# Optimization experiments

Measured on AMD Instinct MI355X. Metric: run time of the kernel, lower is better.

## Reference

```python
import jax, jax.numpy as jnp
import numpy as np

B, D_IN, T = 16, 512, 4096
N_CB, K, D_CB = 9, 1024, 8
EPS = 1e-12  # F.normalize eps


def setup_inputs() -> dict:
    key = jax.random.key(0)
    ks = jax.random.split(key, 8)
    z = jax.random.normal(ks[0], (B, D_IN, T), dtype=jnp.float32)
    # weight-norm params: weight = g * v / ||v|| (norm over all dims except out-channel)
    in_v = jax.random.normal(ks[1], (N_CB, D_CB, D_IN), dtype=jnp.float32) * 0.05
    in_g = jax.random.uniform(ks[2], (N_CB, D_CB), minval=0.5, maxval=1.5, dtype=jnp.float32)
    in_b = jax.random.normal(ks[3], (N_CB, D_CB), dtype=jnp.float32) * 0.01
    out_v = jax.random.normal(ks[4], (N_CB, D_IN, D_CB), dtype=jnp.float32) * 0.05
    out_g = jax.random.uniform(ks[5], (N_CB, D_IN), minval=0.5, maxval=1.5, dtype=jnp.float32)
    out_b = jax.random.normal(ks[6], (N_CB, D_IN), dtype=jnp.float32) * 0.01
    codebooks = jax.random.normal(ks[7], (N_CB, K, D_CB), dtype=jnp.float32)
    return dict(z=z, in_v=in_v, in_g=in_g, in_b=in_b,
                out_v=out_v, out_g=out_g, out_b=out_b, codebooks=codebooks)


def _wn_weight(g, v):
    # weight_norm over dim=0: normalize each output row of v
    return g[:, None] * v / jnp.linalg.norm(v, axis=1, keepdims=True)


def reference(z, in_v, in_g, in_b, out_v, out_g, out_b, codebooks):
    def step(carry, p):
        residual, latent, closs, bloss = carry
        ivi, igi, ibi, ovi, ogi, obi, cb = p
        # in_proj (1x1 conv == channel matmul)
        W_in = _wn_weight(igi, ivi)                               # [d_cb, d_in]
        z_e = jnp.einsum('oc,bct->bot', W_in, residual) + ibi[None, :, None]  # [b, d_cb, t]
        enc = z_e.transpose(0, 2, 1).reshape(B * T, D_CB)         # (b t) d
        enc_n = enc / jnp.maximum(jnp.linalg.norm(enc, axis=1, keepdims=True), EPS)
        cb_n = cb / jnp.maximum(jnp.linalg.norm(cb, axis=1, keepdims=True), EPS)
        # squared L2 distance between normalized vectors
        dist = ((enc_n * enc_n).sum(1, keepdims=True)
                - 2.0 * enc_n @ cb_n.T
                + (cb_n * cb_n).sum(1)[None, :])                  # [(b t), K]
        idx = jnp.argmin(dist, axis=1).reshape(B, T)              # [b, t]
        z_q = cb[idx].transpose(0, 2, 1)                          # [b, d_cb, t] (raw codebook)
        # losses: per-batch mean over [1,2], then mean over batch == global mean (eval mask all True)
        closs = closs + ((z_e - jax.lax.stop_gradient(z_q)) ** 2).mean()
        bloss = bloss + ((z_q - jax.lax.stop_gradient(z_e)) ** 2).mean()
        # straight-through estimator
        z_q_st = z_e + jax.lax.stop_gradient(z_q - z_e)
        W_out = _wn_weight(ogi, ovi)                              # [d_in, d_cb]
        lat_i = jnp.einsum('oc,bct->bot', W_out, z_q_st) + obi[None, :, None]  # [b, d_in, t]
        latent = latent + lat_i
        residual = residual - lat_i
        return (residual, latent, closs, bloss), idx

    init = (z, jnp.zeros_like(z), jnp.float32(0.0), jnp.float32(0.0))
    xs = (in_v, in_g, in_b, out_v, out_g, out_b, codebooks)
    (_, latent, closs, bloss), indices = jax.lax.scan(step, init, xs)
    codes = indices.transpose(1, 0, 2)  # [b, n_codebooks, t]
    return codes, latent, closs, bloss
```

## Files before the change

### kernel.cpp

```cpp
#include <hip/hip_runtime.h>
#include <hip/hip_bf16.h>

constexpr int NB  = 16;
constexpr int DIN = 512;
constexpr int TT  = 4096;
constexpr int NCB = 9;
constexpr int KK  = 1024;

constexpr size_t OUT_LAT   = (size_t)NB * NCB * TT;
constexpr size_t OUT_CLOSS = OUT_LAT + (size_t)NB * DIN * TT;

constexpr int SRES = 514;
constexpr int SWIN = 516;

__device__ __align__(16) float g_cbn [NCB * KK * 8];
__device__ __align__(16) float g_c2  [NCB * KK];
__device__ __align__(16) float g_win [NCB * 8 * DIN];
__device__ __align__(16) float g_wout[NCB * DIN * 8];
__device__ double g_loss;

__device__ __forceinline__ float sqf(float x) {
  float r = x * x;
  asm volatile("" : "+v"(r));
  return r;
}

__global__ void prep_win_k(const float* __restrict__ in_v, const float* __restrict__ in_g) {
  const int r = blockIdx.x * 64 + threadIdx.x;
  if (r >= NCB * 8) return;
  const float* v = in_v + (size_t)r * DIN;
  float blk[4];
#pragma unroll
  for (int bb = 0; bb < 4; ++bb) {
    const float* a = v + bb * 128;
    float r8[8];
#pragma unroll
    for (int j = 0; j < 8; ++j) r8[j] = sqf(a[j]);
#pragma unroll
    for (int m = 1; m < 16; ++m)
#pragma unroll
      for (int j = 0; j < 8; ++j) r8[j] += sqf(a[m * 8 + j]);
    blk[bb] = ((r8[0] + r8[1]) + (r8[2] + r8[3])) + ((r8[4] + r8[5]) + (r8[6] + r8[7]));
  }
  const float total = (blk[0] + blk[1]) + (blk[2] + blk[3]);
  const float nrm = sqrtf(total);
  const float g = in_g[r];
  float* w = g_win + (size_t)r * DIN;
  for (int c = 0; c < DIN; ++c) w[c] = (g * v[c]) / nrm;
}

__global__ void prep_wout_k(const float* __restrict__ out_v, const float* __restrict__ out_g) {
  const int row = blockIdx.x * 256 + threadIdx.x;
  const float* v = out_v + (size_t)row * 8;
  float q[8];
#pragma unroll
  for (int d = 0; d < 8; ++d) q[d] = sqf(v[d]);
  const float nrm = sqrtf(((q[0] + q[1]) + (q[2] + q[3])) + ((q[4] + q[5]) + (q[6] + q[7])));
  const float g = out_g[row];
  float* w = g_wout + (size_t)row * 8;
#pragma unroll
  for (int d = 0; d < 8; ++d) w[d] = (g * v[d]) / nrm;
}

__global__ void prep_cbn_k(const float* __restrict__ cb) {
  const int row = blockIdx.x * 256 + threadIdx.x;
  const float* v = cb + (size_t)row * 8;
  float q[8];
#pragma unroll
  for (int d = 0; d < 8; ++d) q[d] = sqf(v[d]);
  float nrm = sqrtf(((q[0] + q[1]) + (q[2] + q[3])) + ((q[4] + q[5]) + (q[6] + q[7])));
  nrm = fmaxf(nrm, 1e-12f);
  float cn[8];
#pragma unroll
  for (int d = 0; d < 8; ++d) { cn[d] = v[d] / nrm; g_cbn[(size_t)row * 8 + d] = cn[d]; }
  float s2[8];
#pragma unroll
  for (int d = 0; d < 8; ++d) s2[d] = sqf(cn[d]);
  g_c2[row] = ((s2[0] + s2[1]) + (s2[2] + s2[3])) + ((s2[4] + s2[5]) + (s2[6] + s2[7]));
  if (row == 0) g_loss = 0.0;
}

__global__ __launch_bounds__(256, 3)
void rvq_main_k(const float* __restrict__ z, const float* __restrict__ in_b,
                const float* __restrict__ out_b, const float* __restrict__ cb,
                float* __restrict__ out) {
  __shared__ __align__(16) float s_res[16 * SRES];
  __shared__ __align__(16) float s_win[8 * SWIN];
  __shared__ float s_ze[128];
  __shared__ float s_en[128];
  __shared__ float s_s[16];
  __shared__ float s_cd[256];
  __shared__ int   s_ck[256];
  __shared__ float s_zq[128];

  const int tid = threadIdx.x;
  const int col = tid & 15;
  const int grp = tid >> 4;
  const int b   = blockIdx.x >> 8;
  const int t0  = (blockIdx.x & 255) << 4;

  float lr[32];
  {
    const float* zb = z + (size_t)b * DIN * TT + t0 + col;
#pragma unroll
    for (int j = 0; j < 32; ++j) {
      const int c = grp + (j << 4);
      s_res[col * SRES + c] = zb[(size_t)c * TT];
      lr[j] = 0.0f;
    }
  }

  float loss_acc = 0.0f;

  for (int i = 0; i < NCB; ++i) {
    {
      const float4* gw = (const float4*)(g_win + i * 4096);
#pragma unroll
      for (int q = 0; q < 4; ++q) {
        const int e = (q * 256 + tid) * 4;
        *(float4*)(s_win + (e >> 9) * SWIN + (e & 511)) = gw[q * 256 + tid];
      }
    }
    __syncthreads();

    if (tid < 128) {
      const int o = tid >> 4, cc = tid & 15;
      const float2* wr = (const float2*)(s_win + o * SWIN);
      const float2* rr = (const float2*)(s_res + cc * SRES);
      float acc = 0.0f;
#pragma unroll 8
      for (int h = 0; h < 256; ++h) {
        const float2 w = wr[h];
        const float2 r = rr[h];
        acc = fmaf(w.x, r.x, acc);
        acc = fmaf(w.y, r.y, acc);
      }
      s_ze[o * 16 + cc] = acc + in_b[i * 8 + o];
    }
    __syncthreads();

    if (tid < 16) {
      float e[8], q[8];
#pragma unroll
      for (int d = 0; d < 8; ++d) { e[d] = s_ze[d * 16 + tid]; q[d] = sqf(e[d]); }
      float nrm = sqrtf(((q[0] + q[1]) + (q[2] + q[3])) + ((q[4] + q[5]) + (q[6] + q[7])));
      nrm = fmaxf(nrm, 1e-12f);
      float en[8], s2[8];
#pragma unroll
      for (int d = 0; d < 8; ++d) { en[d] = e[d] / nrm; s_en[d * 16 + tid] = en[d]; s2[d] = sqf(en[d]); }
      s_s[tid] = ((s2[0] + s2[1]) + (s2[2] + s2[3])) + ((s2[4] + s2[5]) + (s2[6] + s2[7]));
    }
    __syncthreads();

    {
      const float en0 = s_en[0 * 16 + col], en1 = s_en[1 * 16 + col];
      const float en2 = s_en[2 * 16 + col], en3 = s_en[3 * 16 + col];
      const float en4 = s_en[4 * 16 + col], en5 = s_en[5 * 16 + col];
      const float en6 = s_en[6 * 16 + col], en7 = s_en[7 * 16 + col];
      const float sv = s_s[col];
      const float* cp  = g_cbn + (size_t)i * 8192 + (grp << 3);
      const float* c2p = g_c2 + i * KK + grp;
      float dmin = 3.402823466e38f; int kmin = 0;
#pragma unroll 4
      for (int j = 0; j < 64; ++j) {
        const float4 c0 = *(const float4*)(cp + (j << 7));
        const float4 c1 = *(const float4*)(cp + (j << 7) + 4);
        const float cc2 = c2p[j << 4];
        float dot = 0.0f;
        dot = fmaf(en0, c0.x, dot); dot = fmaf(en1, c0.y, dot);
        dot = fmaf(en2, c0.z, dot); dot = fmaf(en3, c0.w, dot);
        dot = fmaf(en4, c1.x, dot); dot = fmaf(en5, c1.y, dot);
        dot = fmaf(en6, c1.z, dot); dot = fmaf(en7, c1.w, dot);
        const float dist = fmaf(-2.0f, dot, sv) + cc2;
        if (dist < dmin) { dmin = dist; kmin = (j << 4) + grp; }
      }
      s_cd[grp * 16 + col] = dmin;
      s_ck[grp * 16 + col] = kmin;
    }
    __syncthreads();

    if (tid < 16) {
      float bd = s_cd[tid]; int bk = s_ck[tid];
#pragma unroll
      for (int ks = 1; ks < 16; ++ks) {
        const float d2 = s_cd[ks * 16 + tid]; const int k2 = s_ck[ks * 16 + tid];
        if (d2 < bd || (d2 == bd && k2 < bk)) { bd = d2; bk = k2; }
      }
      out[((size_t)b * NCB + i) * TT + t0 + tid] = (float)bk;
      const float* cr = cb + ((size_t)i * KK + bk) * 8;
#pragma unroll
      for (int d = 0; d < 8; ++d) {
        const float zq = cr[d];
        const float ze = s_ze[d * 16 + tid];
        const float df = ze - zq;
        loss_acc = fmaf(df, df, loss_acc);
        s_zq[d * 16 + tid] = ze + (zq - ze);
      }
    }
    __syncthreads();

    {
      const float q0 = s_zq[0 * 16 + col], q1 = s_zq[1 * 16 + col];
      const float q2 = s_zq[2 * 16 + col], q3 = s_zq[3 * 16 + col];
      const float q4 = s_zq[4 * 16 + col], q5 = s_zq[5 * 16 + col];
      const float q6 = s_zq[6 * 16 + col], q7 = s_zq[7 * 16 + col];
      const float* gw = g_wout + (size_t)i * 4096;
      const float* ob = out_b + i * DIN;
#pragma unroll 4
      for (int j = 0; j < 32; ++j) {
        const int c = grp + (j << 4);
        const float4 w0 = *(const float4*)(gw + c * 8);
        const float4 w1 = *(const float4*)(gw + c * 8 + 4);
        float dot = 0.0f;
        dot = fmaf(w0.x, q0, dot); dot = fmaf(w0.y, q1, dot);
        dot = fmaf(w0.z, q2, dot); dot = fmaf(w0.w, q3, dot);
        dot = fmaf(w1.x, q4, dot); dot = fmaf(w1.y, q5, dot);
        dot = fmaf(w1.z, q6, dot); dot = fmaf(w1.w, q7, dot);
        const float lat = dot + ob[c];
        lr[j] += lat;
        s_res[col * SRES + c] -= lat;
      }
    }
  }

  {
    float* lat = out + OUT_LAT;
#pragma unroll
    for (int j = 0; j < 32; ++j) {
      const int c = grp + (j << 4);
      lat[((size_t)b * DIN + c) * TT + t0 + col] = lr[j];
    }
  }

  if (tid < 64) {
    float v = loss_acc;
#pragma unroll
    for (int off = 32; off; off >>= 1) v += __shfl_down(v, off);
    if (tid == 0) atomicAdd(&g_loss, (double)v);
  }
}

__global__ void rvq_epi_k(float* __restrict__ out) {
  const float m = (float)(g_loss / 524288.0);
  out[OUT_CLOSS]     = m;
  out[OUT_CLOSS + 1] = m;
}

extern "C" void kernel_launch(void* const* d_in, const int* in_sizes, int n_in,
                              void* d_out, int out_size, void* d_ws, size_t ws_size,
                              hipStream_t stream) {
  const float* z     = (const float*)d_in[0];
  const float* in_v  = (const float*)d_in[1];
  const float* in_g  = (const float*)d_in[2];
  const float* in_b  = (const float*)d_in[3];
  const float* out_v = (const float*)d_in[4];
  const float* out_g = (const float*)d_in[5];
  const float* out_b = (const float*)d_in[6];
  const float* cb    = (const float*)d_in[7];
  float* out = (float*)d_out;
  (void)d_ws; (void)ws_size;

  prep_win_k <<<2, 64, 0, stream>>>(in_v, in_g);
  prep_wout_k<<<18, 256, 0, stream>>>(out_v, out_g);
  prep_cbn_k <<<36, 256, 0, stream>>>(cb);
  rvq_main_k <<<4096, 256, 0, stream>>>(z, in_b, out_b, cb, out);
  rvq_epi_k  <<<1, 1, 0, stream>>>(out);
}
```

Baseline: 1.432 ms.

## Restructure RVQ block: fewer barriers, shuffle argmin, global W_in reads, fused prep

```diff
diff --git a/kernel.cpp b/kernel.cpp
--- a/kernel.cpp
+++ b/kernel.cpp
@@ -10,8 +10,7 @@
 constexpr size_t OUT_LAT   = (size_t)NB * NCB * TT;
 constexpr size_t OUT_CLOSS = OUT_LAT + (size_t)NB * DIN * TT;
 
-constexpr int SRES = 514;
-constexpr int SWIN = 516;
+constexpr int SRES = 516;
 
 __device__ __align__(16) float g_cbn [NCB * KK * 8];
 __device__ __align__(16) float g_c2  [NCB * KK];
@@ -25,77 +24,75 @@
   return r;
 }
 
-__global__ void prep_win_k(const float* __restrict__ in_v, const float* __restrict__ in_g) {
-  const int r = blockIdx.x * 64 + threadIdx.x;
-  if (r >= NCB * 8) return;
-  const float* v = in_v + (size_t)r * DIN;
-  float blk[4];
-#pragma unroll
-  for (int bb = 0; bb < 4; ++bb) {
-    const float* a = v + bb * 128;
-    float r8[8];
-#pragma unroll
-    for (int j = 0; j < 8; ++j) r8[j] = sqf(a[j]);
-#pragma unroll
-    for (int m = 1; m < 16; ++m)
-#pragma unroll
-      for (int j = 0; j < 8; ++j) r8[j] += sqf(a[m * 8 + j]);
-    blk[bb] = ((r8[0] + r8[1]) + (r8[2] + r8[3])) + ((r8[4] + r8[5]) + (r8[6] + r8[7]));
-  }
-  const float total = (blk[0] + blk[1]) + (blk[2] + blk[3]);
-  const float nrm = sqrtf(total);
-  const float g = in_g[r];
-  float* w = g_win + (size_t)r * DIN;
-  for (int c = 0; c < DIN; ++c) w[c] = (g * v[c]) / nrm;
-}
-
-__global__ void prep_wout_k(const float* __restrict__ out_v, const float* __restrict__ out_g) {
-  const int row = blockIdx.x * 256 + threadIdx.x;
-  const float* v = out_v + (size_t)row * 8;
-  float q[8];
-#pragma unroll
-  for (int d = 0; d < 8; ++d) q[d] = sqf(v[d]);
-  const float nrm = sqrtf(((q[0] + q[1]) + (q[2] + q[3])) + ((q[4] + q[5]) + (q[6] + q[7])));
-  const float g = out_g[row];
-  float* w = g_wout + (size_t)row * 8;
-#pragma unroll
-  for (int d = 0; d < 8; ++d) w[d] = (g * v[d]) / nrm;
-}
-
-__global__ void prep_cbn_k(const float* __restrict__ cb) {
-  const int row = blockIdx.x * 256 + threadIdx.x;
-  const float* v = cb + (size_t)row * 8;
-  float q[8];
-#pragma unroll
-  for (int d = 0; d < 8; ++d) q[d] = sqf(v[d]);
-  float nrm = sqrtf(((q[0] + q[1]) + (q[2] + q[3])) + ((q[4] + q[5]) + (q[6] + q[7])));
-  nrm = fmaxf(nrm, 1e-12f);
-  float cn[8];
-#pragma unroll
-  for (int d = 0; d < 8; ++d) { cn[d] = v[d] / nrm; g_cbn[(size_t)row * 8 + d] = cn[d]; }
-  float s2[8];
-#pragma unroll
-  for (int d = 0; d < 8; ++d) s2[d] = sqf(cn[d]);
-  g_c2[row] = ((s2[0] + s2[1]) + (s2[2] + s2[3])) + ((s2[4] + s2[5]) + (s2[6] + s2[7]));
-  if (row == 0) g_loss = 0.0;
-}
-
-__global__ __launch_bounds__(256, 3)
+__global__ void prep_all_k(const float* __restrict__ in_v, const float* __restrict__ in_g,
+                           const float* __restrict__ out_v, const float* __restrict__ out_g,
+                           const float* __restrict__ cb) {
+  const int bid = blockIdx.x, tid = threadIdx.x;
+  if (bid < 36) {
+    const int row = bid * 256 + tid;
+    const float* v = cb + (size_t)row * 8;
+    float q[8];
+#pragma unroll
+    for (int d = 0; d < 8; ++d) q[d] = sqf(v[d]);
+    float nrm = sqrtf(((q[0] + q[1]) + (q[2] + q[3])) + ((q[4] + q[5]) + (q[6] + q[7])));
+    nrm = fmaxf(nrm, 1e-12f);
+    float cn[8];
+#pragma unroll
+    for (int d = 0; d < 8; ++d) { cn[d] = v[d] / nrm; g_cbn[(size_t)row * 8 + d] = cn[d]; }
+    float s2[8];
+#pragma unroll
+    for (int d = 0; d < 8; ++d) s2[d] = sqf(cn[d]);
+    g_c2[row] = ((s2[0] + s2[1]) + (s2[2] + s2[3])) + ((s2[4] + s2[5]) + (s2[6] + s2[7]));
+    if (row == 0) g_loss = 0.0;
+  } else if (bid < 54) {
+    const int row = (bid - 36) * 256 + tid;
+    const float* v = out_v + (size_t)row * 8;
+    float q[8];
+#pragma unroll
+    for (int d = 0; d < 8; ++d) q[d] = sqf(v[d]);
+    const float nrm = sqrtf(((q[0] + q[1]) + (q[2] + q[3])) + ((q[4] + q[5]) + (q[6] + q[7])));
+    const float g = out_g[row];
+    float* w = g_wout + (size_t)row * 8;
+#pragma unroll
+    for (int d = 0; d < 8; ++d) w[d] = (g * v[d]) / nrm;
+  } else {
+    const int r = tid;
+    if (r >= NCB * 8) return;
+    const float* v = in_v + (size_t)r * DIN;
+    float blk[4];
+#pragma unroll
+    for (int bb = 0; bb < 4; ++bb) {
+      const float* a = v + bb * 128;
+      float r8[8];
+#pragma unroll
+      for (int j = 0; j < 8; ++j) r8[j] = sqf(a[j]);
+#pragma unroll
+      for (int m = 1; m < 16; ++m)
+#pragma unroll
+        for (int j = 0; j < 8; ++j) r8[j] += sqf(a[m * 8 + j]);
+      blk[bb] = ((r8[0] + r8[1]) + (r8[2] + r8[3])) + ((r8[4] + r8[5]) + (r8[6] + r8[7]));
+    }
+    const float total = (blk[0] + blk[1]) + (blk[2] + blk[3]);
+    const float nrm = sqrtf(total);
+    const float g = in_g[r];
+    float* w = g_win + (size_t)r * DIN;
+    for (int c = 0; c < DIN; ++c) w[c] = (g * v[c]) / nrm;
+  }
+}
+
+__global__ __launch_bounds__(256, 4)
 void rvq_main_k(const float* __restrict__ z, const float* __restrict__ in_b,
                 const float* __restrict__ out_b, const float* __restrict__ cb,
                 float* __restrict__ out) {
   __shared__ __align__(16) float s_res[16 * SRES];
-  __shared__ __align__(16) float s_win[8 * SWIN];
   __shared__ float s_ze[128];
-  __shared__ float s_en[128];
-  __shared__ float s_s[16];
-  __shared__ float s_cd[256];
-  __shared__ int   s_ck[256];
   __shared__ float s_zq[128];
 
   const int tid = threadIdx.x;
   const int col = tid & 15;
-  const int grp = tid >> 4;
+  const int cg  = tid >> 4;
+  const int bcol = tid >> 4;
+  const int ksb  = tid & 15;
   const int b   = blockIdx.x >> 8;
   const int t0  = (blockIdx.x & 255) << 4;
 
@@ -103,140 +100,135 @@
   {
     const float* zb = z + (size_t)b * DIN * TT + t0 + col;
 #pragma unroll
-    for (int j = 0; j < 32; ++j) {
-      const int c = grp + (j << 4);
-      s_res[col * SRES + c] = zb[(size_t)c * TT];
-      lr[j] = 0.0f;
+    for (int p = 0; p < 16; ++p) {
+      const int c0 = 2 * cg + 32 * p;
+      const float v0 = zb[(size_t)c0 * TT];
+      const float v1 = zb[(size_t)(c0 + 1) * TT];
+      *(float2*)(s_res + col * SRES + c0) = make_float2(v0, v1);
+      lr[2 * p] = 0.0f; lr[2 * p + 1] = 0.0f;
     }
   }
 
   float loss_acc = 0.0f;
 
   for (int i = 0; i < NCB; ++i) {
+    __syncthreads();
+
+    if (tid < 64) {
+      const int cc = tid & 15, og = tid >> 4;
+      const float4* rr  = (const float4*)(s_res + cc * SRES);
+      const float4* w0p = (const float4*)(g_win + (size_t)(i * 8 + og) * DIN);
+      const float4* w1p = (const float4*)(g_win + (size_t)(i * 8 + og + 4) * DIN);
+      float a0 = 0.0f, a1 = 0.0f;
+#pragma unroll 4
+      for (int h = 0; h < 128; ++h) {
+        const float4 r  = rr[h];
+        const float4 w0 = w0p[h];
+        const float4 w1 = w1p[h];
+        a0 = fmaf(w0.x, r.x, a0); a0 = fmaf(w0.y, r.y, a0);
+        a0 = fmaf(w0.z, r.z, a0); a0 = fmaf(w0.w, r.w, a0);
+        a1 = fmaf(w1.x, r.x, a1); a1 = fmaf(w1.y, r.y, a1);
+        a1 = fmaf(w1.z, r.z, a1); a1 = fmaf(w1.w, r.w, a1);
+      }
+      s_ze[og * 16 + cc]       = a0 + in_b[i * 8 + og];
+      s_ze[(og + 4) * 16 + cc] = a1 + in_b[i * 8 + og + 4];
+    }
+    __syncthreads();
+
     {
-      const float4* gw = (const float4*)(g_win + i * 4096);
-#pragma unroll
-      for (int q = 0; q < 4; ++q) {
-        const int e = (q * 256 + tid) * 4;
-        *(float4*)(s_win + (e >> 9) * SWIN + (e & 511)) = gw[q * 256 + tid];
-      }
-    }
-    __syncthreads();
-
-    if (tid < 128) {
-      const int o = tid >> 4, cc = tid & 15;
-      const float2* wr = (const float2*)(s_win + o * SWIN);
-      const float2* rr = (const float2*)(s_res + cc * SRES);
-      float acc = 0.0f;
-#pragma unroll 8
-      for (int h = 0; h < 256; ++h) {
-        const float2 w = wr[h];
-        const float2 r = rr[h];
-        acc = fmaf(w.x, r.x, acc);
-        acc = fmaf(w.y, r.y, acc);
-      }
-      s_ze[o * 16 + cc] = acc + in_b[i * 8 + o];
-    }
-    __syncthreads();
-
-    if (tid < 16) {
       float e[8], q[8];
 #pragma unroll
-      for (int d = 0; d < 8; ++d) { e[d] = s_ze[d * 16 + tid]; q[d] = sqf(e[d]); }
+      for (int d = 0; d < 8; ++d) { e[d] = s_ze[d * 16 + bcol]; q[d] = sqf(e[d]); }
       float nrm = sqrtf(((q[0] + q[1]) + (q[2] + q[3])) + ((q[4] + q[5]) + (q[6] + q[7])));
       nrm = fmaxf(nrm, 1e-12f);
       float en[8], s2[8];
 #pragma unroll
-      for (int d = 0; d < 8; ++d) { en[d] = e[d] / nrm; s_en[d * 16 + tid] = en[d]; s2[d] = sqf(en[d]); }
-      s_s[tid] = ((s2[0] + s2[1]) + (s2[2] + s2[3])) + ((s2[4] + s2[5]) + (s2[6] + s2[7]));
-    }
-    __syncthreads();
-
-    {
-      const float en0 = s_en[0 * 16 + col], en1 = s_en[1 * 16 + col];
-      const float en2 = s_en[2 * 16 + col], en3 = s_en[3 * 16 + col];
-      const float en4 = s_en[4 * 16 + col], en5 = s_en[5 * 16 + col];
-      const float en6 = s_en[6 * 16 + col], en7 = s_en[7 * 16 + col];
-      const float sv = s_s[col];
-      const float* cp  = g_cbn + (size_t)i * 8192 + (grp << 3);
-      const float* c2p = g_c2 + i * KK + grp;
+      for (int d = 0; d < 8; ++d) { en[d] = e[d] / nrm; s2[d] = sqf(en[d]); }
+      const float sv = ((s2[0] + s2[1]) + (s2[2] + s2[3])) + ((s2[4] + s2[5]) + (s2[6] + s2[7]));
+
+      const float4* cp4 = (const float4*)(g_cbn + (size_t)i * 8192 + (ksb << 3));
+      const float* c2p  = g_c2 + i * KK + ksb;
       float dmin = 3.402823466e38f; int kmin = 0;
 #pragma unroll 4
       for (int j = 0; j < 64; ++j) {
-        const float4 c0 = *(const float4*)(cp + (j << 7));
-        const float4 c1 = *(const float4*)(cp + (j << 7) + 4);
+        const float4 c0 = cp4[j * 32];
+        const float4 c1 = cp4[j * 32 + 1];
         const float cc2 = c2p[j << 4];
         float dot = 0.0f;
-        dot = fmaf(en0, c0.x, dot); dot = fmaf(en1, c0.y, dot);
-        dot = fmaf(en2, c0.z, dot); dot = fmaf(en3, c0.w, dot);
-        dot = fmaf(en4, c1.x, dot); dot = fmaf(en5, c1.y, dot);
-        dot = fmaf(en6, c1.z, dot); dot = fmaf(en7, c1.w, dot);
+        dot = fmaf(en[0], c0.x, dot); dot = fmaf(en[1], c0.y, dot);
+        dot = fmaf(en[2], c0.z, dot); dot = fmaf(en[3], c0.w, dot);
+        dot = fmaf(en[4], c1.x, dot); dot = fmaf(en[5], c1.y, dot);
+        dot = fmaf(en[6], c1.z, dot); dot = fmaf(en[7], c1.w, dot);
         const float dist = fmaf(-2.0f, dot, sv) + cc2;
-        if (dist < dmin) { dmin = dist; kmin = (j << 4) + grp; }
-      }
-      s_cd[grp * 16 + col] = dmin;
-      s_ck[grp * 16 + col] = kmin;
-    }
-    __syncthreads();
-
-    if (tid < 16) {
-      float bd = s_cd[tid]; int bk = s_ck[tid];
-#pragma unroll
-      for (int ks = 1; ks < 16; ++ks) {
-        const float d2 = s_cd[ks * 16 + tid]; const int k2 = s_ck[ks * 16 + tid];
-        if (d2 < bd || (d2 == bd && k2 < bk)) { bd = d2; bk = k2; }
-      }
-      out[((size_t)b * NCB + i) * TT + t0 + tid] = (float)bk;
-      const float* cr = cb + ((size_t)i * KK + bk) * 8;
-#pragma unroll
-      for (int d = 0; d < 8; ++d) {
-        const float zq = cr[d];
-        const float ze = s_ze[d * 16 + tid];
+        if (dist < dmin) { dmin = dist; kmin = (j << 4) + ksb; }
+      }
+#pragma unroll
+      for (int m = 1; m < 16; m <<= 1) {
+        const float od = __shfl_xor(dmin, m, 16);
+        const int   ok = __shfl_xor(kmin, m, 16);
+        if (od < dmin || (od == dmin && ok < kmin)) { dmin = od; kmin = ok; }
+      }
+      if (ksb == 0) out[((size_t)b * NCB + i) * TT + t0 + bcol] = (float)kmin;
+      if (ksb < 8) {
+        const int d = ksb;
+        const float zq = cb[((size_t)i * KK + kmin) * 8 + d];
+        const float ze = s_ze[d * 16 + bcol];
         const float df = ze - zq;
         loss_acc = fmaf(df, df, loss_acc);
-        s_zq[d * 16 + tid] = ze + (zq - ze);
+        s_zq[d * 16 + bcol] = ze + (zq - ze);
       }
     }
     __syncthreads();
 
     {
-      const float q0 = s_zq[0 * 16 + col], q1 = s_zq[1 * 16 + col];
-      const float q2 = s_zq[2 * 16 + col], q3 = s_zq[3 * 16 + col];
-      const float q4 = s_zq[4 * 16 + col], q5 = s_zq[5 * 16 + col];
-      const float q6 = s_zq[6 * 16 + col], q7 = s_zq[7 * 16 + col];
+      float qv[8];
+#pragma unroll
+      for (int d = 0; d < 8; ++d) qv[d] = s_zq[d * 16 + col];
       const float* gw = g_wout + (size_t)i * 4096;
-      const float* ob = out_b + i * DIN;
+      const float2* ob2 = (const float2*)(out_b + i * DIN);
 #pragma unroll 4
-      for (int j = 0; j < 32; ++j) {
-        const int c = grp + (j << 4);
-        const float4 w0 = *(const float4*)(gw + c * 8);
-        const float4 w1 = *(const float4*)(gw + c * 8 + 4);
-        float dot = 0.0f;
-        dot = fmaf(w0.x, q0, dot); dot = fmaf(w0.y, q1, dot);
-        dot = fmaf(w0.z, q2, dot); dot = fmaf(w0.w, q3, dot);
-        dot = fmaf(w1.x, q4, dot); dot = fmaf(w1.y, q5, dot);
-        dot = fmaf(w1.z, q6, dot); dot = fmaf(w1.w, q7, dot);
-        const float lat = dot + ob[c];
-        lr[j] += lat;
-        s_res[col * SRES + c] -= lat;
+      for (int p = 0; p < 16; ++p) {
+        const int c0 = 2 * cg + 32 * p;
+        const float4 wa = *(const float4*)(gw + c0 * 8);
+        const float4 wb = *(const float4*)(gw + c0 * 8 + 4);
+        const float4 wc = *(const float4*)(gw + c0 * 8 + 8);
+        const float4 wd = *(const float4*)(gw + c0 * 8 + 12);
+        float d0 = 0.0f, d1 = 0.0f;
+        d0 = fmaf(wa.x, qv[0], d0); d0 = fmaf(wa.y, qv[1], d0);
+        d0 = fmaf(wa.z, qv[2], d0); d0 = fmaf(wa.w, qv[3], d0);
+        d0 = fmaf(wb.x, qv[4], d0); d0 = fmaf(wb.y, qv[5], d0);
+        d0 = fmaf(wb.z, qv[6], d0); d0 = fmaf(wb.w, qv[7], d0);
+        d1 = fmaf(wc.x, qv[0], d1); d1 = fmaf(wc.y, qv[1], d1);
+        d1 = fmaf(wc.z, qv[2], d1); d1 = fmaf(wc.w, qv[3], d1);
+        d1 = fmaf(wd.x, qv[4], d1); d1 = fmaf(wd.y, qv[5], d1);
+        d1 = fmaf(wd.z, qv[6], d1); d1 = fmaf(wd.w, qv[7], d1);
+        const float2 ob = ob2[cg + 16 * p];
+        const float lat0 = d0 + ob.x;
+        const float lat1 = d1 + ob.y;
+        lr[2 * p] += lat0; lr[2 * p + 1] += lat1;
+        float2* rp = (float2*)(s_res + col * SRES + c0);
+        float2 rv = *rp;
+        rv.x -= lat0; rv.y -= lat1;
+        *rp = rv;
       }
     }
   }
 
   {
-    float* lat = out + OUT_LAT;
-#pragma unroll
-    for (int j = 0; j < 32; ++j) {
-      const int c = grp + (j << 4);
-      lat[((size_t)b * DIN + c) * TT + t0 + col] = lr[j];
-    }
-  }
-
-  if (tid < 64) {
+    float* lat = out + OUT_LAT + (size_t)b * DIN * TT + t0 + col;
+#pragma unroll
+    for (int p = 0; p < 16; ++p) {
+      const int c0 = 2 * cg + 32 * p;
+      lat[(size_t)c0 * TT]       = lr[2 * p];
+      lat[(size_t)(c0 + 1) * TT] = lr[2 * p + 1];
+    }
+  }
+
+  {
     float v = loss_acc;
 #pragma unroll
     for (int off = 32; off; off >>= 1) v += __shfl_down(v, off);
-    if (tid == 0) atomicAdd(&g_loss, (double)v);
+    if ((tid & 63) == 0) atomicAdd(&g_loss, (double)v);
   }
 }
 
@@ -260,9 +252,7 @@
   float* out = (float*)d_out;
   (void)d_ws; (void)ws_size;
 
-  prep_win_k <<<2, 64, 0, stream>>>(in_v, in_g);
-  prep_wout_k<<<18, 256, 0, stream>>>(out_v, out_g);
-  prep_cbn_k <<<36, 256, 0, stream>>>(cb);
+  prep_all_k <<<55, 256, 0, stream>>>(in_v, in_g, out_v, out_g, cb);
   rvq_main_k <<<4096, 256, 0, stream>>>(z, in_b, out_b, cb, out);
   rvq_epi_k  <<<1, 1, 0, stream>>>(out);
 }
```

Measured after the change: 1.806 ms. +26.1%, slower.
